# Optimization experiments

Hardware: AMD Instinct MI355X
Metric: run time of the kernel (lower is better)

The kernel has to match this reference:

```python
import jax, jax.numpy as jnp
import numpy as np

N_NODES = 100000
N_EDGES = 1600000
R_DIM = 8      # radial_embedding_dim (j)
L_DIM = 4      # angular dim (l)
C_DIM = 8      # channel_dim (k)
CUTOFF = 5.5
MP_NORM_FACTOR = 1.0


def setup_inputs() -> dict:
    key = jax.random.key(0)
    k1, k2, k3, k4, k5, k6, k7 = jax.random.split(key, 7)
    node_feat = jax.random.normal(k1, (N_NODES, R_DIM, L_DIM, C_DIM), dtype=jnp.float32)
    edge_lengths = jax.random.uniform(k2, (N_EDGES,), dtype=jnp.float32) * CUTOFF
    radial_cutoff_fn = jax.random.uniform(k3, (N_EDGES,), dtype=jnp.float32)
    edge_index = jax.random.randint(k4, (2, N_EDGES), 0, N_NODES, dtype=jnp.int64)
    prefactor = jax.random.uniform(k5, (R_DIM, C_DIM), dtype=jnp.float32)
    invr0 = (jax.random.uniform(k6, (R_DIM, C_DIM), dtype=jnp.float32) + 0.5) / CUTOFF
    memory_coef = jnp.float32(0.25)
    return {
        "node_feat": node_feat,
        "edge_lengths": edge_lengths,
        "radial_cutoff_fn": radial_cutoff_fn,
        "edge_index": edge_index,
        "prefactor": prefactor,
        "invr0": invr0,
        "memory_coef": memory_coef,
    }


def reference(node_feat, edge_lengths, radial_cutoff_fn, edge_index, prefactor, invr0, memory_coef):
    n_nodes = node_feat.shape[0]
    # radial decay: [E, R, C] = exp(-len * invr0) * prefactor * cutoff_fn
    radial_decay = (
        jnp.exp(-edge_lengths[:, None, None] * invr0)
        * prefactor
        * radial_cutoff_fn[:, None, None]
    )
    # gather sender features [E, R, L, C] and modulate per (edge, radial, channel)
    sender = node_feat[edge_index[0]]
    message = sender * radial_decay[:, :, None, :]
    # scatter-sum messages to receiver nodes
    agg = jax.ops.segment_sum(message, edge_index[1], num_segments=n_nodes)
    return node_feat * memory_coef + agg * MP_NORM_FACTOR
```

## Files before the change

### kernel.cpp

```cpp
#include <hip/hip_runtime.h>
#include <hip/hip_fp16.h>

#define RLC 256
#define SCAN_BLOCK 256
#define SCAN_ITEMS 4

__device__ __forceinline__ unsigned int bfr(float f) {
    unsigned int u = __float_as_uint(f);
    return (u + 0x7fffu + ((u >> 16) & 1u)) >> 16;
}

__global__ __launch_bounds__(256) void cast_kernel(
    const float4* __restrict__ in, uint4* __restrict__ outp, int n8)
{
    int i = blockIdx.x * blockDim.x + threadIdx.x;
    if (i >= n8) return;
    float4 a = in[2 * i];
    float4 b = in[2 * i + 1];
    uint4 r;
    r.x = bfr(a.x) | (bfr(a.y) << 16);
    r.y = bfr(a.z) | (bfr(a.w) << 16);
    r.z = bfr(b.x) | (bfr(b.y) << 16);
    r.w = bfr(b.z) | (bfr(b.w) << 16);
    outp[i] = r;
}


__global__ __launch_bounds__(256) void hist_rank_kernel(
    const int* __restrict__ edge_index, int* __restrict__ counts,
    unsigned char* __restrict__ rank, int n_edges)
{
    int e = blockIdx.x * blockDim.x + threadIdx.x;
    if (e >= n_edges) return;
    int dst = edge_index[n_edges + e];
    int r = atomicAdd(&counts[dst], 1);
    rank[e] = (unsigned char)r;
}

__global__ __launch_bounds__(SCAN_BLOCK) void scan1_kernel(
    const int* __restrict__ in, int* __restrict__ out,
    int* __restrict__ blocksums, int n)
{
    __shared__ int tmp[SCAN_BLOCK];
    int t = threadIdx.x;
    int base = blockIdx.x * SCAN_BLOCK * SCAN_ITEMS + t * SCAN_ITEMS;
    int v[SCAN_ITEMS];
    int tot = 0;
    #pragma unroll
    for (int k = 0; k < SCAN_ITEMS; ++k) {
        int i = base + k;
        v[k] = (i < n) ? in[i] : 0;
        tot += v[k];
    }
    tmp[t] = tot;
    __syncthreads();
    int run = tot;
    for (int d = 1; d < SCAN_BLOCK; d <<= 1) {
        int x = (t >= d) ? tmp[t - d] : 0;
        __syncthreads();
        tmp[t] += x;
        __syncthreads();
    }
    int excl = tmp[t] - run;
    #pragma unroll
    for (int k = 0; k < SCAN_ITEMS; ++k) {
        int i = base + k;
        if (i < n) out[i] = excl;
        excl += v[k];
    }
    if (t == SCAN_BLOCK - 1) blocksums[blockIdx.x] = tmp[t];
}

__global__ __launch_bounds__(SCAN_BLOCK) void scan2_kernel(
    int* __restrict__ blocksums, int nb)
{
    __shared__ int tmp[SCAN_BLOCK];
    int t = threadIdx.x;
    int v = (t < nb) ? blocksums[t] : 0;
    tmp[t] = v;
    __syncthreads();
    for (int d = 1; d < SCAN_BLOCK; d <<= 1) {
        int x = (t >= d) ? tmp[t - d] : 0;
        __syncthreads();
        tmp[t] += x;
        __syncthreads();
    }
    if (t < nb) blocksums[t] = tmp[t] - v;
}

__global__ __launch_bounds__(256) void scan3_kernel(
    int* __restrict__ offsets, const int* __restrict__ blocksums,
    int n, int n_edges)
{
    int i = blockIdx.x * blockDim.x + threadIdx.x;
    if (i == 0) offsets[n] = n_edges;
    if (i >= n) return;
    offsets[i] += blocksums[i / (SCAN_BLOCK * SCAN_ITEMS)];
}

__global__ __launch_bounds__(256) void scatter_rank_kernel(
    const int* __restrict__ edge_index,
    const float* __restrict__ edge_len,
    const float* __restrict__ cutoff_fn,
    const int* __restrict__ offsets,
    const unsigned char* __restrict__ rank,
    int2* __restrict__ payload, int n_edges)
{
    int e = blockIdx.x * blockDim.x + threadIdx.x;
    if (e >= n_edges) return;
    int dst = edge_index[n_edges + e];
    int src = edge_index[e];
    unsigned int hnl = __half_as_ushort(__float2half(-edge_len[e]));
    unsigned int hcf = __half_as_ushort(__float2half(cutoff_fn[e]));
    int pos = offsets[dst] + (int)rank[e];
    payload[pos] = make_int2(src, (int)((hcf << 16) | hnl));
}

__global__ __launch_bounds__(256) void gather_kernel(
    const float* __restrict__ node_feat,
    const unsigned short* __restrict__ nfb,
    const int2* __restrict__ payload,
    const float* __restrict__ prefactor,
    const float* __restrict__ invr0,
    const float* __restrict__ coef_p,
    const int*  __restrict__ offsets,
    float* __restrict__ out,
    int n_nodes)
{
    int tid  = blockIdx.x * blockDim.x + threadIdx.x;
    int node = tid >> 6;
    int lane = threadIdx.x & 63;
    if (node >= n_nodes) return;

    int f0     = lane << 2;
    int rcbase = ((f0 >> 5) << 3) + (f0 & 7);

    const float LOG2E = 1.4426950408889634f;
    float4 iv = *(const float4*)(invr0 + rcbase);
    iv.x *= LOG2E; iv.y *= LOG2E; iv.z *= LOG2E; iv.w *= LOG2E;
    const float4 pf = *(const float4*)(prefactor + rcbase);
    float coef = *coef_p;

    const float4 self = *(const float4*)(node_feat + (long)node * RLC + f0);
    float ax = self.x * coef, ay = self.y * coef,
          az = self.z * coef, aw = self.w * coef;

    int j   = offsets[node];
    int end = offsets[node + 1];

    for (int base = j; base < end; base += 64) {
        int idx = base + lane;
        int2 p = make_int2(0, 0);
        if (idx < end) p = payload[idx];
        int m = end - base;
        if (m > 64) m = 64;
        int psrc = p.x;
        int ppk  = p.y;

        #pragma unroll 4
        for (int it = 0; it < m; ++it) {
            int src = __shfl(psrc, it, 64);
            int pk  = __shfl(ppk,  it, 64);
            float nl = __half2float(__ushort_as_half((unsigned short)(pk & 0xffff)));
            float cf = __half2float(__ushort_as_half((unsigned short)(((unsigned int)pk) >> 16)));
            uint2 raw = *(const uint2*)(nfb + (long)src * RLC + f0);
            float fx = __uint_as_float(raw.x << 16);
            float fy = __uint_as_float(raw.x & 0xffff0000u);
            float fz = __uint_as_float(raw.y << 16);
            float fw = __uint_as_float(raw.y & 0xffff0000u);
            ax += fx * (exp2f(nl * iv.x) * pf.x * cf);
            ay += fy * (exp2f(nl * iv.y) * pf.y * cf);
            az += fz * (exp2f(nl * iv.z) * pf.z * cf);
            aw += fw * (exp2f(nl * iv.w) * pf.w * cf);
        }
    }

    *(float4*)(out + (long)node * RLC + f0) = make_float4(ax, ay, az, aw);
}

__global__ __launch_bounds__(256) void init_out_kernel(
    const float4* __restrict__ nf4, float4* __restrict__ out4,
    const float* __restrict__ coef_p, int n4)
{
    int i = blockIdx.x * blockDim.x + threadIdx.x;
    if (i >= n4) return;
    float c = *coef_p;
    float4 v = nf4[i];
    out4[i] = make_float4(v.x * c, v.y * c, v.z * c, v.w * c);
}

__global__ __launch_bounds__(256) void edge_scatter_kernel(
    const float* __restrict__ node_feat,
    const float* __restrict__ edge_len,
    const float* __restrict__ cutoff_fn,
    const int*  __restrict__ edge_index,
    const float* __restrict__ prefactor,
    const float* __restrict__ invr0,
    float* __restrict__ out, int n_edges)
{
    int tid  = blockIdx.x * blockDim.x + threadIdx.x;
    int e    = tid >> 6;
    int lane = threadIdx.x & 63;
    if (e >= n_edges) return;
    int   src = edge_index[e];
    int   dst = edge_index[n_edges + e];
    float len = edge_len[e];
    float cf  = cutoff_fn[e];
    int f0     = lane << 2;
    int rcbase = ((f0 >> 5) << 3) + (f0 & 7);
    const float4 iv = *(const float4*)(invr0 + rcbase);
    const float4 pf = *(const float4*)(prefactor + rcbase);
    const float4 s  = *(const float4*)(node_feat + (long)src * RLC + f0);
    float nl = -len;
    float* o = out + (long)dst * RLC + f0;
    atomicAdd(o + 0, s.x * __expf(nl * iv.x) * pf.x * cf);
    atomicAdd(o + 1, s.y * __expf(nl * iv.y) * pf.y * cf);
    atomicAdd(o + 2, s.z * __expf(nl * iv.z) * pf.z * cf);
    atomicAdd(o + 3, s.w * __expf(nl * iv.w) * pf.w * cf);
}

extern "C" void kernel_launch(void* const* d_in, const int* in_sizes, int n_in,
                              void* d_out, int out_size, void* d_ws, size_t ws_size,
                              hipStream_t stream) {
    const float* node_feat  = (const float*)d_in[0];
    const float* edge_len   = (const float*)d_in[1];
    const float* cutoff_fn  = (const float*)d_in[2];
    const int*   edge_index = (const int*)d_in[3];
    const float* prefactor  = (const float*)d_in[4];
    const float* invr0      = (const float*)d_in[5];
    const float* coef_p     = (const float*)d_in[6];
    float* out = (float*)d_out;

    const int n_edges = in_sizes[1];
    const int n_feat  = in_sizes[0];
    const int n_nodes = n_feat / RLC;

    const int per_block = SCAN_BLOCK * SCAN_ITEMS;
    const int nb1 = (n_nodes + per_block - 1) / per_block;
    size_t need = (size_t)n_feat * sizeof(unsigned short)
                + (size_t)n_edges * sizeof(int2)
                + ((size_t)(n_nodes + 1) + n_nodes + 256) * sizeof(int)
                + (size_t)n_edges;

    if (ws_size >= need && nb1 <= SCAN_BLOCK) {
        unsigned short* nfb = (unsigned short*)d_ws;
        int2* payload   = (int2*)(nfb + n_feat);
        int* offsets    = (int*)(payload + n_edges);
        int* counts     = offsets + (n_nodes + 1);
        int* blocksums  = counts + n_nodes;
        unsigned char* rank = (unsigned char*)(blocksums + 256);

        int n8 = n_feat / 8;
        cast_kernel<<<(n8 + 255) / 256, 256, 0, stream>>>(
            (const float4*)node_feat, (uint4*)nfb, n8);

        (void)hipMemsetAsync(counts, 0, (size_t)n_nodes * sizeof(int), stream);

        int eg = (n_edges + 255) / 256;
        hist_rank_kernel<<<eg, 256, 0, stream>>>(edge_index, counts, rank, n_edges);

        scan1_kernel<<<nb1, SCAN_BLOCK, 0, stream>>>(counts, offsets, blocksums, n_nodes);
        scan2_kernel<<<1, SCAN_BLOCK, 0, stream>>>(blocksums, nb1);

        int ng = (n_nodes + 255) / 256;
        scan3_kernel<<<ng, 256, 0, stream>>>(offsets, blocksums, n_nodes, n_edges);

        scatter_rank_kernel<<<eg, 256, 0, stream>>>(
            edge_index, edge_len, cutoff_fn, offsets, rank, payload, n_edges);

        long total = (long)n_nodes * 64;
        int gg = (int)((total + 255) / 256);
        gather_kernel<<<gg, 256, 0, stream>>>(
            node_feat, nfb, payload, prefactor, invr0, coef_p, offsets,
            out, n_nodes);
    } else {
        int n4 = n_feat / 4;
        int block = 256;
        init_out_kernel<<<(n4 + block - 1) / block, block, 0, stream>>>(
            (const float4*)node_feat, (float4*)out, coef_p, n4);
        long total_threads = (long)n_edges * 64;
        int grid = (int)((total_threads + block - 1) / block);
        edge_scatter_kernel<<<grid, block, 0, stream>>>(
            node_feat, edge_len, cutoff_fn, edge_index,
            prefactor, invr0, out, n_edges);
    }
}
```

Baseline: 458.5 us.

## Replace CSR scan pipeline with fixed-size per-node buckets plus overflow list

Replaces the histogram, three-pass scan and scatter pipeline with a single build kernel that appends each edge into a fixed 32-slot bucket per destination node, spilling extra edges to an overflow list that a separate kernel handles with atomics. The bf16 node feature copy is transposed so that each lane's four values match the (r,c) layout, and the per-edge weight is computed once per lane using a hardware exp2 intrinsic. This removes several launches and scan passes. The cost is a larger workspace, strided stores for the output, and reliance on node degree (about 16 on average) rarely exceeding 32.

```diff
diff --git a/kernel.cpp b/kernel.cpp
--- a/kernel.cpp
+++ b/kernel.cpp
@@ -2,13 +2,174 @@
 #include <hip/hip_fp16.h>
 
 #define RLC 256
+#define BUCKET 32
+#define OVF_CAP 65536
 #define SCAN_BLOCK 256
 #define SCAN_ITEMS 4
+
+__device__ __forceinline__ float fast_exp2(float x) {
+#if __has_builtin(__builtin_amdgcn_exp2f)
+    return __builtin_amdgcn_exp2f(x);
+#else
+    return __expf(x * 0.6931471805599453f);
+#endif
+}
 
 __device__ __forceinline__ unsigned int bfr(float f) {
     unsigned int u = __float_as_uint(f);
     return (u + 0x7fffu + ((u >> 16) & 1u)) >> 16;
 }
+
+#define LOG2E 1.4426950408889634f
+
+
+__global__ __launch_bounds__(256) void cast_t_kernel(
+    const float4* __restrict__ in, uint2* __restrict__ outp, int nr)
+{
+    int i = blockIdx.x * blockDim.x + threadIdx.x;
+    if (i >= nr) return;
+    const float4* p = in + (size_t)i * 8;
+    float v[32];
+    #pragma unroll
+    for (int q = 0; q < 8; ++q) {
+        float4 t = p[q];
+        v[4*q+0] = t.x; v[4*q+1] = t.y; v[4*q+2] = t.z; v[4*q+3] = t.w;
+    }
+    uint2* o = outp + (size_t)i * 8;
+    #pragma unroll
+    for (int c = 0; c < 8; ++c) {
+        unsigned int lo = bfr(v[0*8+c]) | (bfr(v[1*8+c]) << 16);
+        unsigned int hi = bfr(v[2*8+c]) | (bfr(v[3*8+c]) << 16);
+        o[c] = make_uint2(lo, hi);
+    }
+}
+
+__global__ __launch_bounds__(256) void build_kernel(
+    const int* __restrict__ edge_index,
+    const float* __restrict__ edge_len,
+    const float* __restrict__ cutoff_fn,
+    int* __restrict__ counts,
+    int2* __restrict__ payload,
+    int4* __restrict__ ovf,
+    int* __restrict__ ovf_cnt,
+    int n_edges)
+{
+    int e = blockIdx.x * blockDim.x + threadIdx.x;
+    if (e >= n_edges) return;
+    int dst = edge_index[n_edges + e];
+    int src = edge_index[e];
+    unsigned int hnl = __half_as_ushort(__float2half(-edge_len[e]));
+    unsigned int hcf = __half_as_ushort(__float2half(cutoff_fn[e]));
+    int pk = (int)((hcf << 16) | hnl);
+    int r = atomicAdd(&counts[dst], 1);
+    if (r < BUCKET) {
+        payload[(size_t)dst * BUCKET + r] = make_int2(src, pk);
+    } else {
+        int o = atomicAdd(ovf_cnt, 1);
+        if (o < OVF_CAP) ovf[o] = make_int4(dst, src, pk, 0);
+    }
+}
+
+__global__ __launch_bounds__(256) void gather_bucket_kernel(
+    const float* __restrict__ node_feat,
+    const unsigned short* __restrict__ nfbT,
+    const int2* __restrict__ payload,
+    const float* __restrict__ prefactor,
+    const float* __restrict__ invr0,
+    const float* __restrict__ coef_p,
+    const int* __restrict__ counts,
+    float* __restrict__ out,
+    int n_nodes)
+{
+    __shared__ float4 slot[4][BUCKET];
+    int wave = threadIdx.x >> 6;
+    int lane = threadIdx.x & 63;
+    int node = blockIdx.x * 4 + wave;
+    bool valid = node < n_nodes;
+
+    float iv = invr0[lane] * LOG2E;
+    float pf = prefactor[lane];
+    float coef = *coef_p;
+
+    int r = lane >> 3, c = lane & 7;
+    long obase = (long)node * RLC + r * 32 + c;
+
+    float a0 = 0.f, a1 = 0.f, a2 = 0.f, a3 = 0.f;
+    int m = 0;
+    if (valid) {
+        int deg = counts[node];
+        m = deg < BUCKET ? deg : BUCKET;
+        a0 = node_feat[obase]      * coef;
+        a1 = node_feat[obase + 8]  * coef;
+        a2 = node_feat[obase + 16] * coef;
+        a3 = node_feat[obase + 24] * coef;
+        if (lane < m) {
+            int2 p = payload[(size_t)node * BUCKET + lane];
+            float nl = __half2float(__ushort_as_half((unsigned short)(p.y & 0xffff)));
+            float cf = __half2float(__ushort_as_half((unsigned short)(((unsigned int)p.y) >> 16)));
+            slot[wave][lane] = make_float4(__int_as_float(p.x), nl, cf, 0.f);
+        }
+    }
+    __syncthreads();
+
+    if (valid) {
+        #pragma unroll 4
+        for (int it = 0; it < m; ++it) {
+            float4 s = slot[wave][it];
+            int src = __float_as_int(s.x);
+            float w = fast_exp2(s.y * iv) * pf * s.z;
+            uint2 raw = *(const uint2*)(nfbT + (size_t)src * RLC + lane * 4);
+            float f0 = __uint_as_float(raw.x << 16);
+            float f1 = __uint_as_float(raw.x & 0xffff0000u);
+            float f2 = __uint_as_float(raw.y << 16);
+            float f3 = __uint_as_float(raw.y & 0xffff0000u);
+            a0 += w * f0; a1 += w * f1; a2 += w * f2; a3 += w * f3;
+        }
+        out[obase]      = a0;
+        out[obase + 8]  = a1;
+        out[obase + 16] = a2;
+        out[obase + 24] = a3;
+    }
+}
+
+__global__ __launch_bounds__(256) void ovf_kernel(
+    const unsigned short* __restrict__ nfbT,
+    const float* __restrict__ prefactor,
+    const float* __restrict__ invr0,
+    const int4* __restrict__ ovf,
+    const int* __restrict__ ovf_cnt,
+    float* __restrict__ out)
+{
+    int gtid = blockIdx.x * blockDim.x + threadIdx.x;
+    int wid  = gtid >> 6;
+    int lane = gtid & 63;
+    int nwaves = (gridDim.x * blockDim.x) >> 6;
+    int n = *ovf_cnt;
+    if (n > OVF_CAP) n = OVF_CAP;
+
+    float iv = invr0[lane] * LOG2E;
+    float pf = prefactor[lane];
+    int r = lane >> 3, c = lane & 7;
+
+    for (int i = wid; i < n; i += nwaves) {
+        int4 rec = ovf[i];
+        int dst = rec.x, src = rec.y, pk = rec.z;
+        float nl = __half2float(__ushort_as_half((unsigned short)(pk & 0xffff)));
+        float cf = __half2float(__ushort_as_half((unsigned short)(((unsigned int)pk) >> 16)));
+        float w = fast_exp2(nl * iv) * pf * cf;
+        uint2 raw = *(const uint2*)(nfbT + (size_t)src * RLC + lane * 4);
+        float f0 = __uint_as_float(raw.x << 16);
+        float f1 = __uint_as_float(raw.x & 0xffff0000u);
+        float f2 = __uint_as_float(raw.y << 16);
+        float f3 = __uint_as_float(raw.y & 0xffff0000u);
+        float* o = out + (long)dst * RLC + r * 32 + c;
+        atomicAdd(o,      w * f0);
+        atomicAdd(o + 8,  w * f1);
+        atomicAdd(o + 16, w * f2);
+        atomicAdd(o + 24, w * f3);
+    }
+}
+
 
 __global__ __launch_bounds__(256) void cast_kernel(
     const float4* __restrict__ in, uint4* __restrict__ outp, int n8)
@@ -25,7 +186,6 @@
     outp[i] = r;
 }
 
-
 __global__ __launch_bounds__(256) void hist_rank_kernel(
     const int* __restrict__ edge_index, int* __restrict__ counts,
     unsigned char* __restrict__ rank, int n_edges)
@@ -135,7 +295,6 @@
     int f0     = lane << 2;
     int rcbase = ((f0 >> 5) << 3) + (f0 & 7);
 
-    const float LOG2E = 1.4426950408889634f;
     float4 iv = *(const float4*)(invr0 + rcbase);
     iv.x *= LOG2E; iv.y *= LOG2E; iv.z *= LOG2E; iv.w *= LOG2E;
     const float4 pf = *(const float4*)(prefactor + rcbase);
@@ -168,10 +327,10 @@
             float fy = __uint_as_float(raw.x & 0xffff0000u);
             float fz = __uint_as_float(raw.y << 16);
             float fw = __uint_as_float(raw.y & 0xffff0000u);
-            ax += fx * (exp2f(nl * iv.x) * pf.x * cf);
-            ay += fy * (exp2f(nl * iv.y) * pf.y * cf);
-            az += fz * (exp2f(nl * iv.z) * pf.z * cf);
-            aw += fw * (exp2f(nl * iv.w) * pf.w * cf);
+            ax += fx * (fast_exp2(nl * iv.x) * pf.x * cf);
+            ay += fy * (fast_exp2(nl * iv.y) * pf.y * cf);
+            az += fz * (fast_exp2(nl * iv.z) * pf.z * cf);
+            aw += fw * (fast_exp2(nl * iv.w) * pf.w * cf);
         }
     }
 
@@ -235,14 +394,43 @@
     const int n_feat  = in_sizes[0];
     const int n_nodes = n_feat / RLC;
 
+    size_t need1 = (size_t)n_feat * 2
+                 + (size_t)n_nodes * BUCKET * 8
+                 + (size_t)OVF_CAP * 16
+                 + (size_t)(n_nodes + 1) * 4;
+
     const int per_block = SCAN_BLOCK * SCAN_ITEMS;
     const int nb1 = (n_nodes + per_block - 1) / per_block;
-    size_t need = (size_t)n_feat * sizeof(unsigned short)
-                + (size_t)n_edges * sizeof(int2)
-                + ((size_t)(n_nodes + 1) + n_nodes + 256) * sizeof(int)
-                + (size_t)n_edges;
-
-    if (ws_size >= need && nb1 <= SCAN_BLOCK) {
+    size_t need2 = (size_t)n_feat * 2
+                 + (size_t)n_edges * 8
+                 + ((size_t)(n_nodes + 1) + n_nodes + 256) * 4
+                 + (size_t)n_edges;
+
+    if (ws_size >= need1) {
+        unsigned short* nfbT = (unsigned short*)d_ws;
+        int2* payload = (int2*)(nfbT + n_feat);
+        int4* ovf     = (int4*)(payload + (size_t)n_nodes * BUCKET);
+        int*  counts  = (int*)(ovf + OVF_CAP);
+        int*  ovf_cnt = counts + n_nodes;
+
+        int nr = n_nodes * 8;
+        cast_t_kernel<<<(nr + 255) / 256, 256, 0, stream>>>(
+            (const float4*)node_feat, (uint2*)nfbT, nr);
+
+        (void)hipMemsetAsync(counts, 0, (size_t)(n_nodes + 1) * sizeof(int), stream);
+
+        int eg = (n_edges + 255) / 256;
+        build_kernel<<<eg, 256, 0, stream>>>(
+            edge_index, edge_len, cutoff_fn, counts, payload, ovf, ovf_cnt, n_edges);
+
+        int gg = (n_nodes + 3) / 4;
+        gather_bucket_kernel<<<gg, 256, 0, stream>>>(
+            node_feat, nfbT, payload, prefactor, invr0, coef_p, counts,
+            out, n_nodes);
+
+        ovf_kernel<<<64, 256, 0, stream>>>(
+            nfbT, prefactor, invr0, ovf, ovf_cnt, out);
+    } else if (ws_size >= need2 && nb1 <= SCAN_BLOCK) {
         unsigned short* nfb = (unsigned short*)d_ws;
         int2* payload   = (int2*)(nfb + n_feat);
         int* offsets    = (int*)(payload + n_edges);
@@ -258,13 +446,10 @@
 
         int eg = (n_edges + 255) / 256;
         hist_rank_kernel<<<eg, 256, 0, stream>>>(edge_index, counts, rank, n_edges);
-
         scan1_kernel<<<nb1, SCAN_BLOCK, 0, stream>>>(counts, offsets, blocksums, n_nodes);
         scan2_kernel<<<1, SCAN_BLOCK, 0, stream>>>(blocksums, nb1);
-
         int ng = (n_nodes + 255) / 256;
         scan3_kernel<<<ng, 256, 0, stream>>>(offsets, blocksums, n_nodes, n_edges);
-
         scatter_rank_kernel<<<eg, 256, 0, stream>>>(
             edge_index, edge_len, cutoff_fn, offsets, rank, payload, n_edges);
 
@@ -275,12 +460,11 @@
             out, n_nodes);
     } else {
         int n4 = n_feat / 4;
-        int block = 256;
-        init_out_kernel<<<(n4 + block - 1) / block, block, 0, stream>>>(
+        init_out_kernel<<<(n4 + 255) / 256, 256, 0, stream>>>(
             (const float4*)node_feat, (float4*)out, coef_p, n4);
         long total_threads = (long)n_edges * 64;
-        int grid = (int)((total_threads + block - 1) / block);
-        edge_scatter_kernel<<<grid, block, 0, stream>>>(
+        int grid = (int)((total_threads + 255) / 256);
+        edge_scatter_kernel<<<grid, 256, 0, stream>>>(
             node_feat, edge_len, cutoff_fn, edge_index,
             prefactor, invr0, out, n_edges);
     }
```

Result: faster. 444.1 us (-3.1%).
